# Kernel optimization log

Measured on AMD Instinct MI355X. Metric: run time of the kernel, lower is better.

The kernel has to match this reference:

```python
import jax, jax.numpy as jnp
import numpy as np


def setup_inputs() -> dict:
    key = jax.random.key(0)
    k1, k2 = jax.random.split(key)
    B, N, M, D = 8, 4096, 4096, 3
    return {
        "input": jax.random.normal(k1, (B, N, D), dtype=jnp.float32),
        "target": jax.random.normal(k2, (B, M, D), dtype=jnp.float32),
    }


def reference(input, target):
    x2 = jnp.sum(input * input, axis=-1)          # [B, N]
    y2 = jnp.sum(target * target, axis=-1)        # [B, M]
    xy = jnp.einsum("bnd,bmd->bnm", input, target)  # [B, N, M]
    sqdist = x2[:, :, None] + y2[:, None, :] - 2.0 * xy
    sqdist = jnp.maximum(sqdist, 0.0)  # clamp numerical negatives
    sqdist1 = jnp.min(sqdist, axis=2)  # nearest target for each input point [B, N]
    sqdist2 = jnp.min(sqdist, axis=1)  # nearest input for each target point [B, M]
    return jnp.mean(sqdist1) + jnp.mean(sqdist2)
```

## Files before the change

### kernel.cpp

```cpp
#include <hip/hip_runtime.h>
#include <math.h>

#define BATCH  8
#define NPTS   4096
#define TPB    256
#define QPT    8
#define QCHUNK (TPB * QPT)
#define NQC    (NPTS / QCHUNK)
#define NCC    32
#define CTILE  (NPTS / NCC)

__global__ __launch_bounds__(TPB) void chamfer_min_kernel(
    const float* __restrict__ input,
    const float* __restrict__ target,
    float* __restrict__ part)
{
    const int dir = blockIdx.z;
    const int b   = blockIdx.y;
    const int qc  = blockIdx.x & (NQC - 1);
    const int cc  = blockIdx.x >> 1;

    const float* __restrict__ qp = (dir ? target : input) + (size_t)b * NPTS * 3;
    const float* __restrict__ cp = (dir ? input  : target) + (size_t)b * NPTS * 3;

    __shared__ float4 cand[CTILE];
    if (threadIdx.x < CTILE) {
        const int c = cc * CTILE + threadIdx.x;
        const float cx = cp[3 * c + 0];
        const float cy = cp[3 * c + 1];
        const float cz = cp[3 * c + 2];
        cand[threadIdx.x] = make_float4(-2.0f * cx, -2.0f * cy, -2.0f * cz,
                                        fmaf(cx, cx, fmaf(cy, cy, cz * cz)));
    }

    const int q0 = qc * QCHUNK + (int)threadIdx.x * QPT;
    float v[3 * QPT];
    const float4* __restrict__ qv = (const float4*)(qp + 3 * q0);
    #pragma unroll
    for (int i = 0; i < 6; ++i) {
        const float4 t = qv[i];
        v[4 * i + 0] = t.x; v[4 * i + 1] = t.y;
        v[4 * i + 2] = t.z; v[4 * i + 3] = t.w;
    }
    float px[QPT], py[QPT], pz[QPT], pmin[QPT];
    #pragma unroll
    for (int k = 0; k < QPT; ++k) {
        px[k] = v[3 * k + 0];
        py[k] = v[3 * k + 1];
        pz[k] = v[3 * k + 2];
        pmin[k] = 3.4e38f;
    }
    __syncthreads();

    #pragma unroll 8
    for (int m = 0; m < CTILE; ++m) {
        const float4 c = cand[m];
        #pragma unroll
        for (int k = 0; k < QPT; ++k) {
            const float t = fmaf(px[k], c.x,
                            fmaf(py[k], c.y,
                            fmaf(pz[k], c.z, c.w)));
            pmin[k] = fminf(pmin[k], t);
        }
    }

    float res[QPT];
    #pragma unroll
    for (int k = 0; k < QPT; ++k) {
        const float x2 = fmaf(px[k], px[k], fmaf(py[k], py[k], pz[k] * pz[k]));
        res[k] = fmaxf(pmin[k] + x2, 0.0f);
    }
    float* o = part + (((size_t)(dir * BATCH + b) * NCC + cc) * NPTS + q0);
    *(float4*)(o + 0) = make_float4(res[0], res[1], res[2], res[3]);
    *(float4*)(o + 4) = make_float4(res[4], res[5], res[6], res[7]);
}

__global__ __launch_bounds__(TPB) void chamfer_reduce_kernel(
    const float* __restrict__ part, float* __restrict__ out)
{
    const int i = (blockIdx.x * TPB + (int)threadIdx.x) * 4;
    const int g = i >> 12;
    const int q = i & (NPTS - 1);
    const float* __restrict__ p = part + ((size_t)g * NCC) * NPTS + q;

    float4 mn = *(const float4*)p;
    #pragma unroll 8
    for (int cc = 1; cc < NCC; ++cc) {
        const float4 t = *(const float4*)(p + (size_t)cc * NPTS);
        mn.x = fminf(mn.x, t.x); mn.y = fminf(mn.y, t.y);
        mn.z = fminf(mn.z, t.z); mn.w = fminf(mn.w, t.w);
    }
    float s = mn.x + mn.y + mn.z + mn.w;
    #pragma unroll
    for (int off = 32; off > 0; off >>= 1)
        s += __shfl_down(s, off, 64);

    __shared__ float wsum[TPB / 64];
    if ((threadIdx.x & 63) == 0) wsum[threadIdx.x >> 6] = s;
    __syncthreads();
    if (threadIdx.x == 0) {
        const float t = wsum[0] + wsum[1] + wsum[2] + wsum[3];
        atomicAdd(out, t * (1.0f / (float)(BATCH * NPTS)));
    }
}

extern "C" void kernel_launch(void* const* d_in, const int* in_sizes, int n_in,
                              void* d_out, int out_size, void* d_ws, size_t ws_size,
                              hipStream_t stream) {
    const float* input  = (const float*)d_in[0];
    const float* target = (const float*)d_in[1];
    float* out  = (float*)d_out;
    float* part = (float*)d_ws;

    hipMemsetAsync(out, 0, sizeof(float), stream);

    dim3 grid1(NQC * NCC, BATCH, 2);
    chamfer_min_kernel<<<grid1, dim3(TPB), 0, stream>>>(input, target, part);

    dim3 grid2((2 * BATCH * NPTS) / (TPB * 4));
    chamfer_reduce_kernel<<<grid2, dim3(TPB), 0, stream>>>(part, out);
}
```

Measured before the change: 81.86 us.

## Compute pairwise distances with bf16 MFMA using hi/lo split precision

Replaces the scalar FMA distance loop with 32x32x16 bf16 MFMA instructions. Coordinates are split into high and low bf16 parts so the dot product plus the squared norm keep close to fp32 accuracy. The partial tiling changes to 4 candidate chunks and 256-row blocks, and the query-norm add and clamp move into the reduce kernel. Row minima come from cross-lane shuffles after each MFMA pass. The split-bf16 scheme drops the lo*lo terms, which risks small numerical error, and the shuffle reductions add overhead.

Result: faster. 75.33 us (-8.0%).

```diff
diff --git a/kernel.cpp b/kernel.cpp
--- a/kernel.cpp
+++ b/kernel.cpp
@@ -1,122 +1,175 @@
 #include <hip/hip_runtime.h>
 #include <math.h>
 
-#define BATCH  8
-#define NPTS   4096
-#define TPB    256
-#define QPT    8
-#define QCHUNK (TPB * QPT)
-#define NQC    (NPTS / QCHUNK)
-#define NCC    32
-#define CTILE  (NPTS / NCC)
+#define BATCH 8
+#define NPTS  4096
+#define TPB   256
+#define NCC   4
+#define CHUNK (NPTS / NCC)
+#define ROWS  256
+#define NRC   (NPTS / ROWS)
+#define WROWS 64
 
-__global__ __launch_bounds__(TPB) void chamfer_min_kernel(
+typedef __bf16 bf16x8 __attribute__((ext_vector_type(8)));
+typedef float  f32x16 __attribute__((ext_vector_type(16)));
+
+__global__ __launch_bounds__(TPB) void chamfer_mfma_kernel(
     const float* __restrict__ input,
     const float* __restrict__ target,
     float* __restrict__ part)
 {
-    const int dir = blockIdx.z;
-    const int b   = blockIdx.y;
-    const int qc  = blockIdx.x & (NQC - 1);
-    const int cc  = blockIdx.x >> 1;
+  const int dir = blockIdx.z, b = blockIdx.y;
+  const int rc = blockIdx.x & (NRC - 1);
+  const int cc = blockIdx.x >> 4;
 
-    const float* __restrict__ qp = (dir ? target : input) + (size_t)b * NPTS * 3;
-    const float* __restrict__ cp = (dir ? input  : target) + (size_t)b * NPTS * 3;
+  const float* __restrict__ qp = (dir ? target : input) + (size_t)b * NPTS * 3;
+  const float* __restrict__ cp = (dir ? input  : target) + (size_t)b * NPTS * 3;
 
-    __shared__ float4 cand[CTILE];
-    if (threadIdx.x < CTILE) {
-        const int c = cc * CTILE + threadIdx.x;
-        const float cx = cp[3 * c + 0];
-        const float cy = cp[3 * c + 1];
-        const float cz = cp[3 * c + 2];
-        cand[threadIdx.x] = make_float4(-2.0f * cx, -2.0f * cy, -2.0f * cz,
-                                        fmaf(cx, cx, fmaf(cy, cy, cz * cz)));
+  __shared__ bf16x8 sB[2][CHUNK];
+  __shared__ bf16x8 sA[2][ROWS];
+
+  {
+    const int c0 = cc * CHUNK + (int)threadIdx.x * 4;
+    const float4* __restrict__ cv = (const float4*)(cp + 3 * c0);
+    const float4 f0 = cv[0], f1 = cv[1], f2 = cv[2];
+    float xs[4] = { f0.x, f0.w, f1.z, f2.y };
+    float ys[4] = { f0.y, f1.x, f1.w, f2.z };
+    float zs[4] = { f0.z, f1.y, f2.x, f2.w };
+    #pragma unroll
+    for (int j = 0; j < 4; ++j) {
+      const float mx = -2.f * xs[j], my = -2.f * ys[j], mz = -2.f * zs[j];
+      const __bf16 hx = (__bf16)mx, hy = (__bf16)my, hz = (__bf16)mz;
+      const __bf16 lx = (__bf16)(mx - (float)hx);
+      const __bf16 ly = (__bf16)(my - (float)hy);
+      const __bf16 lz = (__bf16)(mz - (float)hz);
+      const float y2 = fmaf(xs[j], xs[j], fmaf(ys[j], ys[j], zs[j] * zs[j]));
+      const __bf16 h2 = (__bf16)y2, l2 = (__bf16)(y2 - (float)h2);
+      const __bf16 z0 = (__bf16)0.f;
+      bf16x8 v0, v1;
+      v0[0]=hx; v0[1]=hy; v0[2]=hz; v0[3]=lx; v0[4]=ly; v0[5]=lz; v0[6]=z0; v0[7]=z0;
+      v1[0]=hx; v1[1]=hy; v1[2]=hz; v1[3]=h2; v1[4]=l2; v1[5]=z0; v1[6]=z0; v1[7]=z0;
+      sB[0][threadIdx.x * 4 + j] = v0;
+      sB[1][threadIdx.x * 4 + j] = v1;
     }
+  }
+  {
+    const int r = rc * ROWS + (int)threadIdx.x;
+    const float qx = qp[3*r], qy = qp[3*r+1], qz = qp[3*r+2];
+    const __bf16 hx = (__bf16)qx, hy = (__bf16)qy, hz = (__bf16)qz;
+    const __bf16 lx = (__bf16)(qx - (float)hx);
+    const __bf16 ly = (__bf16)(qy - (float)hy);
+    const __bf16 lz = (__bf16)(qz - (float)hz);
+    const __bf16 z0 = (__bf16)0.f, o1 = (__bf16)1.f;
+    bf16x8 v0, v1;
+    v0[0]=hx; v0[1]=hy; v0[2]=hz; v0[3]=hx; v0[4]=hy; v0[5]=hz; v0[6]=z0; v0[7]=z0;
+    v1[0]=lx; v1[1]=ly; v1[2]=lz; v1[3]=o1; v1[4]=o1; v1[5]=z0; v1[6]=z0; v1[7]=z0;
+    sA[0][threadIdx.x] = v0;
+    sA[1][threadIdx.x] = v1;
+  }
+  __syncthreads();
 
-    const int q0 = qc * QCHUNK + (int)threadIdx.x * QPT;
-    float v[3 * QPT];
-    const float4* __restrict__ qv = (const float4*)(qp + 3 * q0);
+  const int lane = (int)threadIdx.x & 63;
+  const int wave = (int)threadIdx.x >> 6;
+  const int half = lane >> 5;
+  const int l31  = lane & 31;
+
+  const bf16x8 a0 = sA[half][wave * WROWS + l31];
+  const bf16x8 a1 = sA[half][wave * WROWS + 32 + l31];
+
+  float rm0[16], rm1[16];
+  #pragma unroll
+  for (int i = 0; i < 16; ++i) { rm0[i] = 3.4e38f; rm1[i] = 3.4e38f; }
+
+  f32x16 zacc;
+  #pragma unroll
+  for (int i = 0; i < 16; ++i) zacc[i] = 0.f;
+
+  #pragma unroll 2
+  for (int m = 0; m < CHUNK / 32; ++m) {
+    const bf16x8 bf = sB[half][m * 32 + l31];
+    const f32x16 d0 = __builtin_amdgcn_mfma_f32_32x32x16_bf16(a0, bf, zacc, 0, 0, 0);
+    const f32x16 d1 = __builtin_amdgcn_mfma_f32_32x32x16_bf16(a1, bf, zacc, 0, 0, 0);
     #pragma unroll
-    for (int i = 0; i < 6; ++i) {
-        const float4 t = qv[i];
-        v[4 * i + 0] = t.x; v[4 * i + 1] = t.y;
-        v[4 * i + 2] = t.z; v[4 * i + 3] = t.w;
+    for (int i = 0; i < 16; ++i) {
+      rm0[i] = fminf(rm0[i], d0[i]);
+      rm1[i] = fminf(rm1[i], d1[i]);
     }
-    float px[QPT], py[QPT], pz[QPT], pmin[QPT];
+  }
+
+  float* __restrict__ po = part +
+      (((size_t)(dir * BATCH + b) * NCC + cc) * NPTS) + rc * ROWS + wave * WROWS;
+  #pragma unroll
+  for (int r = 0; r < 16; ++r) {
+    float v0 = rm0[r], v1 = rm1[r];
     #pragma unroll
-    for (int k = 0; k < QPT; ++k) {
-        px[k] = v[3 * k + 0];
-        py[k] = v[3 * k + 1];
-        pz[k] = v[3 * k + 2];
-        pmin[k] = 3.4e38f;
+    for (int mk = 1; mk < 32; mk <<= 1) {
+      v0 = fminf(v0, __shfl_xor(v0, mk, 64));
+      v1 = fminf(v1, __shfl_xor(v1, mk, 64));
     }
-    __syncthreads();
-
-    #pragma unroll 8
-    for (int m = 0; m < CTILE; ++m) {
-        const float4 c = cand[m];
-        #pragma unroll
-        for (int k = 0; k < QPT; ++k) {
-            const float t = fmaf(px[k], c.x,
-                            fmaf(py[k], c.y,
-                            fmaf(pz[k], c.z, c.w)));
-            pmin[k] = fminf(pmin[k], t);
-        }
+    if (l31 == 0) {
+      const int row = (r & 3) + 8 * (r >> 2) + 4 * half;
+      po[row]      = v0;
+      po[row + 32] = v1;
     }
-
-    float res[QPT];
-    #pragma unroll
-    for (int k = 0; k < QPT; ++k) {
-        const float x2 = fmaf(px[k], px[k], fmaf(py[k], py[k], pz[k] * pz[k]));
-        res[k] = fmaxf(pmin[k] + x2, 0.0f);
-    }
-    float* o = part + (((size_t)(dir * BATCH + b) * NCC + cc) * NPTS + q0);
-    *(float4*)(o + 0) = make_float4(res[0], res[1], res[2], res[3]);
-    *(float4*)(o + 4) = make_float4(res[4], res[5], res[6], res[7]);
+  }
 }
 
 __global__ __launch_bounds__(TPB) void chamfer_reduce_kernel(
-    const float* __restrict__ part, float* __restrict__ out)
+    const float* __restrict__ part,
+    const float* __restrict__ input,
+    const float* __restrict__ target,
+    float* __restrict__ out)
 {
-    const int i = (blockIdx.x * TPB + (int)threadIdx.x) * 4;
-    const int g = i >> 12;
-    const int q = i & (NPTS - 1);
-    const float* __restrict__ p = part + ((size_t)g * NCC) * NPTS + q;
+  const int i = (blockIdx.x * TPB + (int)threadIdx.x) * 4;
+  const int g = i >> 12;
+  const int q = i & (NPTS - 1);
+  const int dir = g >> 3, b = g & 7;
 
-    float4 mn = *(const float4*)p;
-    #pragma unroll 8
-    for (int cc = 1; cc < NCC; ++cc) {
-        const float4 t = *(const float4*)(p + (size_t)cc * NPTS);
-        mn.x = fminf(mn.x, t.x); mn.y = fminf(mn.y, t.y);
-        mn.z = fminf(mn.z, t.z); mn.w = fminf(mn.w, t.w);
-    }
-    float s = mn.x + mn.y + mn.z + mn.w;
-    #pragma unroll
-    for (int off = 32; off > 0; off >>= 1)
-        s += __shfl_down(s, off, 64);
+  const float* __restrict__ p = part + ((size_t)g * NCC) * NPTS + q;
+  float4 mn = *(const float4*)p;
+  #pragma unroll
+  for (int cc = 1; cc < NCC; ++cc) {
+    const float4 t = *(const float4*)(p + (size_t)cc * NPTS);
+    mn.x = fminf(mn.x, t.x); mn.y = fminf(mn.y, t.y);
+    mn.z = fminf(mn.z, t.z); mn.w = fminf(mn.w, t.w);
+  }
+  const float* __restrict__ qp =
+      (dir ? target : input) + (size_t)b * NPTS * 3 + 3 * q;
+  const float4* __restrict__ qv = (const float4*)qp;
+  const float4 a = qv[0], c = qv[1], e = qv[2];
+  const float x20 = fmaf(a.x, a.x, fmaf(a.y, a.y, a.z * a.z));
+  const float x21 = fmaf(a.w, a.w, fmaf(c.x, c.x, c.y * c.y));
+  const float x22 = fmaf(c.z, c.z, fmaf(c.w, c.w, e.x * e.x));
+  const float x23 = fmaf(e.y, e.y, fmaf(e.z, e.z, e.w * e.w));
 
-    __shared__ float wsum[TPB / 64];
-    if ((threadIdx.x & 63) == 0) wsum[threadIdx.x >> 6] = s;
-    __syncthreads();
-    if (threadIdx.x == 0) {
-        const float t = wsum[0] + wsum[1] + wsum[2] + wsum[3];
-        atomicAdd(out, t * (1.0f / (float)(BATCH * NPTS)));
-    }
+  float s = fmaxf(mn.x + x20, 0.f) + fmaxf(mn.y + x21, 0.f) +
+            fmaxf(mn.z + x22, 0.f) + fmaxf(mn.w + x23, 0.f);
+  #pragma unroll
+  for (int off = 32; off > 0; off >>= 1)
+    s += __shfl_down(s, off, 64);
+
+  __shared__ float wsum[TPB / 64];
+  if ((threadIdx.x & 63) == 0) wsum[threadIdx.x >> 6] = s;
+  __syncthreads();
+  if (threadIdx.x == 0) {
+    const float t = wsum[0] + wsum[1] + wsum[2] + wsum[3];
+    atomicAdd(out, t * (1.0f / (float)(BATCH * NPTS)));
+  }
 }
 
 extern "C" void kernel_launch(void* const* d_in, const int* in_sizes, int n_in,
                               void* d_out, int out_size, void* d_ws, size_t ws_size,
                               hipStream_t stream) {
-    const float* input  = (const float*)d_in[0];
-    const float* target = (const float*)d_in[1];
-    float* out  = (float*)d_out;
-    float* part = (float*)d_ws;
+  const float* input  = (const float*)d_in[0];
+  const float* target = (const float*)d_in[1];
+  float* out  = (float*)d_out;
+  float* part = (float*)d_ws;
 
-    hipMemsetAsync(out, 0, sizeof(float), stream);
+  hipMemsetAsync(out, 0, sizeof(float), stream);
 
-    dim3 grid1(NQC * NCC, BATCH, 2);
-    chamfer_min_kernel<<<grid1, dim3(TPB), 0, stream>>>(input, target, part);
+  dim3 grid1(NRC * NCC, BATCH, 2);
+  chamfer_mfma_kernel<<<grid1, dim3(TPB), 0, stream>>>(input, target, part);
 
-    dim3 grid2((2 * BATCH * NPTS) / (TPB * 4));
-    chamfer_reduce_kernel<<<grid2, dim3(TPB), 0, stream>>>(part, out);
+  dim3 grid2((2 * BATCH * NPTS) / (TPB * 4));
+  chamfer_reduce_kernel<<<grid2, dim3(TPB), 0, stream>>>(part, input, target, out);
 }
```
